# Performance work log

Measured on AMD Instinct MI355X. Metric: run time of the kernel, lower is better.

## Reference

```python
import jax, jax.numpy as jnp
import numpy as np

NEG_SLOPE = 0.2  # PyG GATConv default negative_slope


def gat_conv(x, W, b, a_src, a_dst, src, dst, N, H, C):
    """PyG-style GATConv (v1 attention), concat heads, self-loops already in (src,dst)."""
    h = (x @ W).reshape(N, H, C)                       # [N,H,C]
    al_src = jnp.sum(h * a_src, axis=-1)               # [N,H]
    al_dst = jnp.sum(h * a_dst, axis=-1)               # [N,H]
    e = jax.nn.leaky_relu(al_src[src] + al_dst[dst], NEG_SLOPE)  # [E,H]
    m = jax.ops.segment_max(e, dst, num_segments=N)    # segment softmax (stable)
    m = jnp.where(jnp.isfinite(m), m, 0.0)
    ex = jnp.exp(e - m[dst])
    denom = jax.ops.segment_sum(ex, dst, num_segments=N)
    alpha = ex / (denom[dst] + 1e-16)                  # [E,H]
    msg = h[src] * alpha[..., None]                    # [E,H,C]
    out = jax.ops.segment_sum(msg, dst, num_segments=N)  # [N,H,C]
    return out.reshape(N, H * C) + b


def setup_inputs() -> dict:
    key = jax.random.key(0)
    ks = jax.random.split(key, 16)
    N, E, IN, HID, HEADS, OUT, G = 50000, 600000, 128, 64, 4, 10, 64
    x = jax.random.normal(ks[0], (N, IN), dtype=jnp.float32)
    edge_index = jax.random.randint(ks[1], (2, E), 0, N, dtype=jnp.int32)
    batch = jnp.sort(jax.random.randint(ks[2], (N,), 0, G, dtype=jnp.int32))
    s = 0.1
    p = {
        'W1': jax.random.normal(ks[3], (IN, HEADS * HID)) * s,
        'b1': jnp.zeros((HEADS * HID,), jnp.float32),
        'asrc1': jax.random.normal(ks[4], (HEADS, HID)) * s,
        'adst1': jax.random.normal(ks[5], (HEADS, HID)) * s,
        'W2': jax.random.normal(ks[6], (HEADS * HID, HEADS * HID)) * s,
        'b2': jnp.zeros((HEADS * HID,), jnp.float32),
        'asrc2': jax.random.normal(ks[7], (HEADS, HID)) * s,
        'adst2': jax.random.normal(ks[8], (HEADS, HID)) * s,
        'W3': jax.random.normal(ks[9], (HEADS * HID, HID)) * s,
        'b3': jnp.zeros((HID,), jnp.float32),
        'asrc3': jax.random.normal(ks[10], (1, HID)) * s,
        'adst3': jax.random.normal(ks[11], (1, HID)) * s,
        'linW': jax.random.normal(ks[12], (HID, OUT)) * s,
        'linb': jnp.zeros((OUT,), jnp.float32),
    }
    return dict(x=x, edge_index=edge_index, batch=batch, **p)


def reference(x, edge_index, batch, W1, b1, asrc1, adst1, W2, b2, asrc2, adst2,
              W3, b3, asrc3, adst3, linW, linb):
    N = x.shape[0]
    G = 64  # number of graphs
    loops = jnp.arange(N, dtype=edge_index.dtype)
    src = jnp.concatenate([edge_index[0], loops])  # PyG adds self-loops by default
    dst = jnp.concatenate([edge_index[1], loops])
    # eval mode: dropout is identity
    h = jax.nn.elu(gat_conv(x, W1, b1, asrc1, adst1, src, dst, N, 4, 64))
    h = jax.nn.elu(gat_conv(h, W2, b2, asrc2, adst2, src, dst, N, 4, 64))
    h = jax.nn.elu(gat_conv(h, W3, b3, asrc3, adst3, src, dst, N, 1, 64))
    # global mean pool over graphs
    sums = jax.ops.segment_sum(h, batch, num_segments=G)            # [G,64]
    cnts = jax.ops.segment_sum(jnp.ones((N,), h.dtype), batch, num_segments=G)
    pooled = sums / jnp.maximum(cnts, 1.0)[:, None]
    return pooled @ linW + linb                                      # [G,10]
```

## Files before the change

### kernel.cpp

```cpp
#include <hip/hip_runtime.h>
#include <hip/hip_bf16.h>
#include <math.h>

#define NEG_SLOPE 0.2f

typedef short short8 __attribute__((ext_vector_type(8)));
typedef float f32x4 __attribute__((ext_vector_type(4)));
typedef unsigned int u32;
typedef unsigned short u16;

__device__ __forceinline__ float lrelu(float x){ return x > 0.f ? x : NEG_SLOPE * x; }
__device__ __forceinline__ float elu_f(float x){ return x > 0.f ? x : __expf(x) - 1.f; }
__device__ __forceinline__ float blo(u32 w){ return __uint_as_float(w << 16); }
__device__ __forceinline__ float bhi(u32 w){ return __uint_as_float(w & 0xffff0000u); }
__device__ __forceinline__ float bf2f(u16 u){ return __uint_as_float(((u32)u) << 16); }
__device__ __forceinline__ u16 f2bf(float f){
  __hip_bfloat16 h = __float2bfloat16(f);
  return *(u16*)&h;
}

__global__ void prep_kernel(const float* __restrict__ x, u16* __restrict__ xb, int n4,
                            const float* __restrict__ W1, u16* __restrict__ w1t,
                            const float* __restrict__ W2, u16* __restrict__ w2t,
                            const float* __restrict__ W3, u16* __restrict__ w3t,
                            int* __restrict__ cursor, int N,
                            float* __restrict__ sums, int* __restrict__ cnts){
  int i = blockIdx.x * 256 + threadIdx.x;
  if (i < n4){
    float4 v = ((const float4*)x)[i];
    ushort4 o;
    o.x = f2bf(v.x); o.y = f2bf(v.y); o.z = f2bf(v.z); o.w = f2bf(v.w);
    ((ushort4*)xb)[i] = o;
    return;
  }
  int t = i - n4;
  if (t < 128 * 256){
    int k = t >> 8, m = t & 255;
    w1t[m * 128 + k] = f2bf(W1[t]);
    return;
  }
  t -= 128 * 256;
  if (t < 256 * 256){
    int k = t >> 8, m = t & 255;
    w2t[m * 256 + k] = f2bf(W2[t]);
    return;
  }
  t -= 256 * 256;
  if (t < 256 * 64){
    int k = t >> 6, m = t & 63;
    w3t[m * 256 + k] = f2bf(W3[t]);
    return;
  }
  t -= 256 * 64;
  if (t < N){ cursor[t] = 0; return; }
  t -= N;
  if (t < 64 * 64){ sums[t] = 0.f; return; }
  t -= 64 * 64;
  if (t < 64) cnts[t] = 0;
}

__global__ void ell_kernel(const int* __restrict__ src, const int* __restrict__ dst,
                           int E, int* cursor, int* __restrict__ ell){
  int i = blockIdx.x * 256 + threadIdx.x;
  if (i < E){
    int s = src[i], d = dst[i];
    int pos = atomicAdd(&cursor[d], 1);
    if (pos < 64) ell[(size_t)d * 64 + pos] = s;
  }
}

template<int BN>
__global__ __launch_bounds__((BN == 256) ? 512 : 256) void gemm_mfma(
    const u16* __restrict__ A, const u16* __restrict__ Bt, u16* __restrict__ C,
    const float* __restrict__ asrc, const float* __restrict__ adst,
    float* __restrict__ als, float* __restrict__ ald, int N, int K, int M){
  constexpr int T  = (BN == 256) ? 512 : 256;
  constexpr int MI = (BN == 256) ? 4 : 2;
  constexpr int HH = BN / 64;
  constexpr int AQ = 1024 / T;
  constexpr int SB = BN * 8 / T;
  constexpr int LB = (BN == 256) ? 8 : 6;
  __shared__ short As[8][128][8];
  __shared__ short Bs[8][BN][8];
  const int tid = threadIdx.x;
  const int w = tid >> 6, lane = tid & 63;
  const int quad = lane >> 4, l16 = lane & 15;
  const int row0 = blockIdx.y * 128;
  const int wrow = (BN == 256) ? (w >> 2) * 64 : w * 32;
  const int wcol = (BN == 256) ? (w & 3) * 64 : 0;

  f32x4 acc[MI][4];
#pragma unroll
  for (int i = 0; i < MI; i++)
#pragma unroll
    for (int j = 0; j < 4; j++) acc[i][j] = (f32x4){0.f, 0.f, 0.f, 0.f};

  for (int k0 = 0; k0 < K; k0 += 64){
    __syncthreads();
#pragma unroll
    for (int q = 0; q < AQ; q++){
      int lb = q * T + w * 64;
      int li = lb + lane;
      int c = li >> 7, r = li & 127;
      int grow = min(row0 + r, N - 1);
      const u16* gp = A + (size_t)grow * K + k0 + c * 8;
      __builtin_amdgcn_global_load_lds((const __attribute__((address_space(1))) void*)gp,
                                       (__attribute__((address_space(3))) void*)((char*)&As[0][0][0] + (size_t)lb * 16),
                                       16, 0, 0);
    }
#pragma unroll
    for (int q = 0; q < SB; q++){
      int lb = q * T + w * 64;
      int li = lb + lane;
      int c = li >> LB, n = li & (BN - 1);
      const u16* gp = Bt + (size_t)n * K + k0 + c * 8;
      __builtin_amdgcn_global_load_lds((const __attribute__((address_space(1))) void*)gp,
                                       (__attribute__((address_space(3))) void*)((char*)&Bs[0][0][0] + (size_t)lb * 16),
                                       16, 0, 0);
    }
    __syncthreads();
#pragma unroll
    for (int ks = 0; ks < 2; ks++){
      short8 a[MI], b[4];
#pragma unroll
      for (int i = 0; i < MI; i++) a[i] = *(const short8*)&As[ks * 4 + quad][wrow + i * 16 + l16][0];
#pragma unroll
      for (int j = 0; j < 4; j++)  b[j] = *(const short8*)&Bs[ks * 4 + quad][wcol + j * 16 + l16][0];
#pragma unroll
      for (int i = 0; i < MI; i++)
#pragma unroll
        for (int j = 0; j < 4; j++)
          acc[i][j] = __builtin_amdgcn_mfma_f32_16x16x32_bf16(a[i], b[j], acc[i][j], 0, 0, 0);
    }
  }

  const int head = wcol >> 6;
  float avs[4], avd[4];
#pragma unroll
  for (int j = 0; j < 4; j++){
    int c = j * 16 + l16;
    avs[j] = asrc[head * 64 + c];
    avd[j] = adst[head * 64 + c];
  }

#pragma unroll
  for (int i = 0; i < MI; i++){
#pragma unroll
    for (int rr = 0; rr < 4; rr++){
      int row = row0 + wrow + i * 16 + quad * 4 + rr;
      float ps = acc[i][0][rr] * avs[0] + acc[i][1][rr] * avs[1]
               + acc[i][2][rr] * avs[2] + acc[i][3][rr] * avs[3];
      float pd = acc[i][0][rr] * avd[0] + acc[i][1][rr] * avd[1]
               + acc[i][2][rr] * avd[2] + acc[i][3][rr] * avd[3];
#pragma unroll
      for (int off = 8; off > 0; off >>= 1){
        ps += __shfl_xor(ps, off);
        pd += __shfl_xor(pd, off);
      }
      if (row < N){
#pragma unroll
        for (int j = 0; j < 4; j++)
          C[(size_t)row * M + wcol + j * 16 + l16] = f2bf(acc[i][j][rr]);
        if (l16 == 0){
          als[(size_t)row * HH + head] = ps;
          ald[(size_t)row * HH + head] = pd;
        }
      }
    }
  }
}

__global__ __launch_bounds__(256) void agg4_kernel(const u16* __restrict__ hb,
    const float* __restrict__ als, const float* __restrict__ ald,
    const int* __restrict__ degv, const int* __restrict__ ell,
    const float* __restrict__ bias, u16* __restrict__ out, int N){
  __shared__ float lex[4][256];
  __shared__ int lu[4][64];
  int wslot = threadIdx.x >> 6;
  int node = (blockIdx.x * 256 + threadIdx.x) >> 6;
  int lane = threadIdx.x & 63;
  if (node >= N) return;
  int deg = min(degv[node], 64);
  float4 t4 = *(const float4*)(ald + node * 4);
  const int hh = lane >> 4;

  bool v = lane < deg;
  int u = v ? ell[(size_t)node * 64 + lane] : 0;
  float4 s = *(const float4*)(als + (size_t)u * 4);
  float4 exv;
  exv.x = v ? __expf(lrelu(s.x + t4.x)) : 0.f;
  exv.y = v ? __expf(lrelu(s.y + t4.y)) : 0.f;
  exv.z = v ? __expf(lrelu(s.z + t4.z)) : 0.f;
  exv.w = v ? __expf(lrelu(s.w + t4.w)) : 0.f;
  *(float4*)&lex[wslot][lane * 4] = exv;
  lu[wslot][lane] = u;
  asm volatile("s_waitcnt lgkmcnt(0)" ::: "memory");

  const u16* hbl = hb + lane * 4;
  float4 ss = *(const float4*)(als + (size_t)node * 4);
  float es0 = __expf(lrelu(ss.x + t4.x));
  float es1 = __expf(lrelu(ss.y + t4.y));
  float es2 = __expf(lrelu(ss.z + t4.z));
  float es3 = __expf(lrelu(ss.w + t4.w));
  float exs = (hh == 0) ? es0 : (hh == 1) ? es1 : (hh == 2) ? es2 : es3;
  uint2 tself = *(const uint2*)(hbl + (size_t)node * 256);
  float denom = exs;
  float a0 = exs * blo(tself.x), a1 = exs * bhi(tself.x);
  float a2 = exs * blo(tself.y), a3 = exs * bhi(tself.y);

#pragma unroll 8
  for (int jj = 0; jj < deg; jj++){
    float ex = lex[wslot][jj * 4 + hh];
    int uu = lu[wslot][jj];
    uint2 t = *(const uint2*)(hbl + (size_t)uu * 256);
    denom += ex;
    a0 += ex * blo(t.x);
    a1 += ex * bhi(t.x);
    a2 += ex * blo(t.y);
    a3 += ex * bhi(t.y);
  }
  float inv = 1.f / (denom + 1e-16f);
  int ch = lane * 4;
  float o0 = elu_f(a0 * inv + bias[ch]);
  float o1 = elu_f(a1 * inv + bias[ch + 1]);
  float o2 = elu_f(a2 * inv + bias[ch + 2]);
  float o3 = elu_f(a3 * inv + bias[ch + 3]);
  uint2 o;
  o.x = (u32)f2bf(o0) | ((u32)f2bf(o1) << 16);
  o.y = (u32)f2bf(o2) | ((u32)f2bf(o3) << 16);
  ((uint2*)out)[(size_t)node * 64 + lane] = o;
}

__global__ __launch_bounds__(256) void agg1_kernel(const u16* __restrict__ hb,
    const float* __restrict__ als, const float* __restrict__ ald,
    const int* __restrict__ degv, const int* __restrict__ ell,
    const float* __restrict__ bias, u16* __restrict__ out, int N){
  __shared__ float lex[4][72];
  __shared__ int lu[4][72];
  int wslot = threadIdx.x >> 6;
  int node = (blockIdx.x * 256 + threadIdx.x) >> 6;
  int lane = threadIdx.x & 63;
  if (node >= N) return;
  int deg = min(degv[node], 64);
  float adv = ald[node];

  bool v = lane < deg;
  int u = v ? ell[(size_t)node * 64 + lane] : 0;
  lex[wslot][lane] = v ? __expf(lrelu(als[u] + adv)) : 0.f;
  lu[wslot][lane] = u;
  if (lane < 8){ lex[wslot][64 + lane] = 0.f; lu[wslot][64 + lane] = 0; }
  asm volatile("s_waitcnt lgkmcnt(0)" ::: "memory");

  int eo = lane >> 4;
  int chb = (lane & 15) * 4;
  float a0 = 0.f, a1 = 0.f, a2 = 0.f, a3 = 0.f, denom = 0.f;
  if (eo == 0){
    float exs = __expf(lrelu(als[node] + adv));
    uint2 t = *(const uint2*)(hb + (size_t)node * 64 + chb);
    denom = exs;
    a0 = exs * blo(t.x); a1 = exs * bhi(t.x);
    a2 = exs * blo(t.y); a3 = exs * bhi(t.y);
  }
#pragma unroll 4
  for (int j2 = 0; j2 < deg; j2 += 4){
    int jj = j2 + eo;
    float ex = lex[wslot][jj];
    int uu = lu[wslot][jj];
    uint2 t = *(const uint2*)(hb + (size_t)uu * 64 + chb);
    denom += ex;
    a0 += ex * blo(t.x);
    a1 += ex * bhi(t.x);
    a2 += ex * blo(t.y);
    a3 += ex * bhi(t.y);
  }
#pragma unroll
  for (int off = 16; off < 64; off <<= 1){
    denom += __shfl_xor(denom, off);
    a0 += __shfl_xor(a0, off); a1 += __shfl_xor(a1, off);
    a2 += __shfl_xor(a2, off); a3 += __shfl_xor(a3, off);
  }
  if (eo == 0){
    float inv = 1.f / (denom + 1e-16f);
    float o0 = elu_f(a0 * inv + bias[chb]);
    float o1 = elu_f(a1 * inv + bias[chb + 1]);
    float o2 = elu_f(a2 * inv + bias[chb + 2]);
    float o3 = elu_f(a3 * inv + bias[chb + 3]);
    uint2 o;
    o.x = (u32)f2bf(o0) | ((u32)f2bf(o1) << 16);
    o.y = (u32)f2bf(o2) | ((u32)f2bf(o3) << 16);
    *(uint2*)(out + (size_t)node * 64 + chb) = o;
  }
}

__global__ void pool_kernel(const u16* __restrict__ f, const int* __restrict__ batch,
                            float* sums, int* cnts, int N){
  int lane = threadIdx.x;
  int s = blockIdx.x * 128;
  if (s >= N) return;
  int e = min(s + 128, N);
  float acc = 0.f;
  int cnt = 0;
  int cur = batch[s];
  for (int n = s; n < e; n++){
    int g = batch[n];
    if (g != cur){
      atomicAdd(&sums[cur * 64 + lane], acc);
      if (lane == 0) atomicAdd(&cnts[cur], cnt);
      acc = 0.f; cnt = 0; cur = g;
    }
    acc += bf2f(f[(size_t)n * 64 + lane]);
    cnt++;
  }
  atomicAdd(&sums[cur * 64 + lane], acc);
  if (lane == 0) atomicAdd(&cnts[cur], cnt);
}

__global__ void final_kernel(const float* __restrict__ sums, const int* __restrict__ cnts,
                             const float* __restrict__ linW, const float* __restrict__ linb,
                             float* __restrict__ out){
  int t = threadIdx.x;
  if (t >= 640) return;
  int g = t / 10, o = t % 10;
  float c = fmaxf((float)cnts[g], 1.f);
  float acc = 0.f;
#pragma unroll
  for (int k = 0; k < 64; k++) acc += sums[g * 64 + k] * linW[k * 10 + o];
  out[t] = acc / c + linb[o];
}

extern "C" void kernel_launch(void* const* d_in, const int* in_sizes, int n_in,
                              void* d_out, int out_size, void* d_ws, size_t ws_size,
                              hipStream_t stream) {
  const float* x     = (const float*)d_in[0];
  const int*   ei    = (const int*)  d_in[1];
  const int*   batch = (const int*)  d_in[2];
  const float* W1    = (const float*)d_in[3];
  const float* b1    = (const float*)d_in[4];
  const float* asrc1 = (const float*)d_in[5];
  const float* adst1 = (const float*)d_in[6];
  const float* W2    = (const float*)d_in[7];
  const float* b2    = (const float*)d_in[8];
  const float* asrc2 = (const float*)d_in[9];
  const float* adst2 = (const float*)d_in[10];
  const float* W3    = (const float*)d_in[11];
  const float* b3    = (const float*)d_in[12];
  const float* asrc3 = (const float*)d_in[13];
  const float* adst3 = (const float*)d_in[14];
  const float* linW  = (const float*)d_in[15];
  const float* linb  = (const float*)d_in[16];

  const int N = in_sizes[0] / 128;
  const int E = in_sizes[1] / 2;
  const int G = 64;
  const int* src = ei;
  const int* dst = ei + E;

  char* p = (char*)d_ws;
  auto carve = [&](size_t bytes) -> char* {
    char* r = p;
    p += (bytes + 255) & ~(size_t)255;
    return r;
  };
  u16*   xb       = (u16*)  carve((size_t)N * 128 * 2);
  u16*   w1t      = (u16*)  carve((size_t)256 * 128 * 2);
  u16*   w2t      = (u16*)  carve((size_t)256 * 256 * 2);
  u16*   w3t      = (u16*)  carve((size_t)64 * 256 * 2);
  u16*   hb       = (u16*)  carve((size_t)N * 256 * 2);
  u16*   featb    = (u16*)  carve((size_t)N * 256 * 2);
  u16*   out3     = (u16*)  carve((size_t)N * 64 * 2);
  float* als      = (float*)carve((size_t)N * 4 * 4);
  float* ald      = (float*)carve((size_t)N * 4 * 4);
  int*   cursor   = (int*)  carve((size_t)N * 4);
  int*   ell      = (int*)  carve((size_t)N * 64 * 4);
  float* sums     = (float*)carve((size_t)G * 64 * 4);
  int*   cnts     = (int*)  carve((size_t)G * 4);

  const int n4 = N * 128 / 4;
  const int prep_items = n4 + 128 * 256 + 256 * 256 + 256 * 64 + N + G * 64 + G;

  prep_kernel<<<(prep_items + 255) / 256, 256, 0, stream>>>(x, xb, n4, W1, w1t, W2, w2t, W3, w3t,
                                                            cursor, N, sums, cnts);

  ell_kernel<<<(E + 255) / 256, 256, 0, stream>>>(src, dst, E, cursor, ell);

  const int nby = (N + 127) / 128;
  const int wpn_grid = (N + 3) / 4;

  gemm_mfma<256><<<dim3(1, nby), 512, 0, stream>>>(xb, w1t, hb, asrc1, adst1, als, ald, N, 128, 256);
  agg4_kernel<<<wpn_grid, 256, 0, stream>>>(hb, als, ald, cursor, ell, b1, featb, N);

  gemm_mfma<256><<<dim3(1, nby), 512, 0, stream>>>(featb, w2t, hb, asrc2, adst2, als, ald, N, 256, 256);
  agg4_kernel<<<wpn_grid, 256, 0, stream>>>(hb, als, ald, cursor, ell, b2, featb, N);

  gemm_mfma<64><<<dim3(1, nby), 256, 0, stream>>>(featb, w3t, hb, asrc3, adst3, als, ald, N, 256, 64);
  agg1_kernel<<<wpn_grid, 256, 0, stream>>>(hb, als, ald, cursor, ell, b3, out3, N);

  pool_kernel<<<(N + 127) / 128, 64, 0, stream>>>(out3, batch, sums, cnts, N);
  final_kernel<<<1, 640, 0, stream>>>(sums, cnts, linW, linb, (float*)d_out);
}
```

Before: 368.3 us.

## Store GEMM output in 32-channel slices and split aggregation across slices

The 256-wide GEMMs now write hidden features in a sliced layout, where each 32-channel slice is a contiguous N×32 array. The aggregation kernel becomes eight blocks per group of nodes, one per slice. Each wave processes four edges at a time, with 16 lanes per edge reading 64 bytes, and the partial sums are combined with shuffles. The goal is to keep each slice's gather working set small enough to stay cache-resident and to improve gather locality. In exchange, the edge list and attention values are reloaded eight times per node, exp work is repeated across slices, and only a quarter of the lanes do the final write.

```diff
diff --git a/kernel.cpp b/kernel.cpp
--- a/kernel.cpp
+++ b/kernel.cpp
@@ -69,7 +69,7 @@
   }
 }
 
-template<int BN>
+template<int BN, bool SLICED>
 __global__ __launch_bounds__((BN == 256) ? 512 : 256) void gemm_mfma(
     const u16* __restrict__ A, const u16* __restrict__ Bt, u16* __restrict__ C,
     const float* __restrict__ asrc, const float* __restrict__ adst,
@@ -159,8 +159,13 @@
       }
       if (row < N){
 #pragma unroll
-        for (int j = 0; j < 4; j++)
-          C[(size_t)row * M + wcol + j * 16 + l16] = f2bf(acc[i][j][rr]);
+        for (int j = 0; j < 4; j++){
+          int col = wcol + j * 16 + l16;
+          if (SLICED)
+            C[((size_t)(col >> 5) * N + row) * 32 + (col & 31)] = f2bf(acc[i][j][rr]);
+          else
+            C[(size_t)row * M + col] = f2bf(acc[i][j][rr]);
+        }
         if (l16 == 0){
           als[(size_t)row * HH + head] = ps;
           ald[(size_t)row * HH + head] = pd;
@@ -170,65 +175,63 @@
   }
 }
 
-__global__ __launch_bounds__(256) void agg4_kernel(const u16* __restrict__ hb,
+__global__ __launch_bounds__(256) void agg4s_kernel(const u16* __restrict__ hb,
     const float* __restrict__ als, const float* __restrict__ ald,
     const int* __restrict__ degv, const int* __restrict__ ell,
     const float* __restrict__ bias, u16* __restrict__ out, int N){
-  __shared__ float lex[4][256];
+  __shared__ float lex[4][64];
   __shared__ int lu[4][64];
-  int wslot = threadIdx.x >> 6;
-  int node = (blockIdx.x * 256 + threadIdx.x) >> 6;
-  int lane = threadIdx.x & 63;
+  const int slice = blockIdx.x & 7;
+  const int wslot = threadIdx.x >> 6;
+  const int node = (blockIdx.x >> 3) * 4 + wslot;
+  const int lane = threadIdx.x & 63;
   if (node >= N) return;
+  const int head = slice >> 1;
+  const int eo = lane >> 4;
+  const int cl = lane & 15;
+  const int cb = slice * 32 + cl * 2;
+  const u16* hs = hb + (size_t)slice * N * 32;
+
   int deg = min(degv[node], 64);
-  float4 t4 = *(const float4*)(ald + node * 4);
-  const int hh = lane >> 4;
+  float adh = ald[node * 4 + head];
 
   bool v = lane < deg;
-  int u = v ? ell[(size_t)node * 64 + lane] : 0;
-  float4 s = *(const float4*)(als + (size_t)u * 4);
-  float4 exv;
-  exv.x = v ? __expf(lrelu(s.x + t4.x)) : 0.f;
-  exv.y = v ? __expf(lrelu(s.y + t4.y)) : 0.f;
-  exv.z = v ? __expf(lrelu(s.z + t4.z)) : 0.f;
-  exv.w = v ? __expf(lrelu(s.w + t4.w)) : 0.f;
-  *(float4*)&lex[wslot][lane * 4] = exv;
+  int u = v ? ell[(size_t)node * 64 + lane] : node;
+  lex[wslot][lane] = v ? __expf(lrelu(als[u * 4 + head] + adh)) : 0.f;
   lu[wslot][lane] = u;
   asm volatile("s_waitcnt lgkmcnt(0)" ::: "memory");
 
-  const u16* hbl = hb + lane * 4;
-  float4 ss = *(const float4*)(als + (size_t)node * 4);
-  float es0 = __expf(lrelu(ss.x + t4.x));
-  float es1 = __expf(lrelu(ss.y + t4.y));
-  float es2 = __expf(lrelu(ss.z + t4.z));
-  float es3 = __expf(lrelu(ss.w + t4.w));
-  float exs = (hh == 0) ? es0 : (hh == 1) ? es1 : (hh == 2) ? es2 : es3;
-  uint2 tself = *(const uint2*)(hbl + (size_t)node * 256);
-  float denom = exs;
-  float a0 = exs * blo(tself.x), a1 = exs * bhi(tself.x);
-  float a2 = exs * blo(tself.y), a3 = exs * bhi(tself.y);
-
-#pragma unroll 8
-  for (int jj = 0; jj < deg; jj++){
-    float ex = lex[wslot][jj * 4 + hh];
+  float denom = 0.f, a0 = 0.f, a1 = 0.f;
+  if (eo == 0){
+    float exs = __expf(lrelu(als[(size_t)node * 4 + head] + adh));
+    u32 t = *(const u32*)(hs + (size_t)node * 32 + cl * 2);
+    denom = exs;
+    a0 = exs * blo(t);
+    a1 = exs * bhi(t);
+  }
+#pragma unroll 4
+  for (int j2 = 0; j2 < deg; j2 += 4){
+    int jj = j2 + eo;
+    float ex = lex[wslot][jj];
     int uu = lu[wslot][jj];
-    uint2 t = *(const uint2*)(hbl + (size_t)uu * 256);
+    u32 t = *(const u32*)(hs + (size_t)uu * 32 + cl * 2);
     denom += ex;
-    a0 += ex * blo(t.x);
-    a1 += ex * bhi(t.x);
-    a2 += ex * blo(t.y);
-    a3 += ex * bhi(t.y);
-  }
-  float inv = 1.f / (denom + 1e-16f);
-  int ch = lane * 4;
-  float o0 = elu_f(a0 * inv + bias[ch]);
-  float o1 = elu_f(a1 * inv + bias[ch + 1]);
-  float o2 = elu_f(a2 * inv + bias[ch + 2]);
-  float o3 = elu_f(a3 * inv + bias[ch + 3]);
-  uint2 o;
-  o.x = (u32)f2bf(o0) | ((u32)f2bf(o1) << 16);
-  o.y = (u32)f2bf(o2) | ((u32)f2bf(o3) << 16);
-  ((uint2*)out)[(size_t)node * 64 + lane] = o;
+    a0 += ex * blo(t);
+    a1 += ex * bhi(t);
+  }
+#pragma unroll
+  for (int off = 16; off < 64; off <<= 1){
+    denom += __shfl_xor(denom, off);
+    a0 += __shfl_xor(a0, off);
+    a1 += __shfl_xor(a1, off);
+  }
+  if (eo == 0){
+    float inv = 1.f / (denom + 1e-16f);
+    float o0 = elu_f(a0 * inv + bias[cb]);
+    float o1 = elu_f(a1 * inv + bias[cb + 1]);
+    u32 o = (u32)f2bf(o0) | ((u32)f2bf(o1) << 16);
+    *(u32*)(out + (size_t)node * 256 + cb) = o;
+  }
 }
 
 __global__ __launch_bounds__(256) void agg1_kernel(const u16* __restrict__ hb,
@@ -384,16 +387,16 @@
   ell_kernel<<<(E + 255) / 256, 256, 0, stream>>>(src, dst, E, cursor, ell);
 
   const int nby = (N + 127) / 128;
-  const int wpn_grid = (N + 3) / 4;
-
-  gemm_mfma<256><<<dim3(1, nby), 512, 0, stream>>>(xb, w1t, hb, asrc1, adst1, als, ald, N, 128, 256);
-  agg4_kernel<<<wpn_grid, 256, 0, stream>>>(hb, als, ald, cursor, ell, b1, featb, N);
-
-  gemm_mfma<256><<<dim3(1, nby), 512, 0, stream>>>(featb, w2t, hb, asrc2, adst2, als, ald, N, 256, 256);
-  agg4_kernel<<<wpn_grid, 256, 0, stream>>>(hb, als, ald, cursor, ell, b2, featb, N);
-
-  gemm_mfma<64><<<dim3(1, nby), 256, 0, stream>>>(featb, w3t, hb, asrc3, adst3, als, ald, N, 256, 64);
-  agg1_kernel<<<wpn_grid, 256, 0, stream>>>(hb, als, ald, cursor, ell, b3, out3, N);
+  const int agg4_grid = 8 * ((N + 3) / 4);
+
+  gemm_mfma<256, true><<<dim3(1, nby), 512, 0, stream>>>(xb, w1t, hb, asrc1, adst1, als, ald, N, 128, 256);
+  agg4s_kernel<<<agg4_grid, 256, 0, stream>>>(hb, als, ald, cursor, ell, b1, featb, N);
+
+  gemm_mfma<256, true><<<dim3(1, nby), 512, 0, stream>>>(featb, w2t, hb, asrc2, adst2, als, ald, N, 256, 256);
+  agg4s_kernel<<<agg4_grid, 256, 0, stream>>>(hb, als, ald, cursor, ell, b2, featb, N);
+
+  gemm_mfma<64, false><<<dim3(1, nby), 256, 0, stream>>>(featb, w3t, hb, asrc3, adst3, als, ald, N, 256, 64);
+  agg1_kernel<<<(N + 3) / 4, 256, 0, stream>>>(hb, als, ald, cursor, ell, b3, out3, N);
 
   pool_kernel<<<(N + 127) / 128, 64, 0, stream>>>(out3, batch, sums, cnts, N);
   final_kernel<<<1, 640, 0, stream>>>(sums, cnts, linW, linb, (float*)d_out);
```

Result: slower. 557.6 us (+51.4%).
